# Optimization experiments

Hardware: AMD Instinct MI355X
Metric: run time of the kernel (lower is better)

Reference implementation:

```python
import jax, jax.numpy as jnp
import numpy as np

N, E, IN_C, OUT_C = 100000, 3200000, 128, 32
NEG_SLOPE = 0.2  # PyG GATConv default negative_slope


def setup_inputs() -> dict:
    key = jax.random.key(0)
    ks = jax.random.split(key, 5)
    x = jax.random.normal(ks[0], (N, IN_C), dtype=jnp.float32)
    edge_index = jax.random.randint(ks[1], (2, E), 0, N, dtype=jnp.int32)
    W = jax.random.normal(ks[2], (IN_C, OUT_C), dtype=jnp.float32) * (1.0 / np.sqrt(IN_C))
    att_src = jax.random.normal(ks[3], (OUT_C,), dtype=jnp.float32) * 0.1
    att_dst = jax.random.normal(ks[4], (OUT_C,), dtype=jnp.float32) * 0.1
    bias = jnp.zeros((OUT_C,), dtype=jnp.float32)
    return {"x": x, "edge_index": edge_index, "W": W,
            "att_src": att_src, "att_dst": att_dst, "bias": bias}


def reference(x, edge_index, W, att_src, att_dst, bias):
    # GATConv (heads=1, concat=True, add_self_loops=True) followed by ReLU.
    n = x.shape[0]
    loops = jnp.arange(n, dtype=edge_index.dtype)
    src = jnp.concatenate([edge_index[0], loops])  # [E+N]
    dst = jnp.concatenate([edge_index[1], loops])  # [E+N]

    h = x @ W                       # [N, C] transformed features
    a_src = h @ att_src             # [N] source attention logits
    a_dst = h @ att_dst             # [N] destination attention logits

    # per-edge unnormalized attention
    e = jax.nn.leaky_relu(a_src[src] + a_dst[dst], NEG_SLOPE)  # [E+N]

    # segment softmax over incoming edges of each destination node
    m = jnp.full((n,), -jnp.inf, dtype=e.dtype).at[dst].max(e)  # per-dst max
    p = jnp.exp(e - m[dst])
    denom = jax.ops.segment_sum(p, dst, num_segments=n)
    alpha = p / denom[dst]          # [E+N]

    # scatter-aggregate weighted messages
    out = jax.ops.segment_sum(alpha[:, None] * h[src], dst, num_segments=n)  # [N, C]
    out = jax.nn.relu(out + bias)
    return (out, edge_index)
```

## Files before the change

kernel.cpp:

```cpp
#include <hip/hip_runtime.h>

#define IN_C 128
#define OUT_C 32
#define NEG_SLOPE 0.2f

#define NBUK 512
#define DRANGE 256
#define STILE 8192
#define HST (STILE / 2)
#define CAP 8192
#define RPT (CAP / 1024)

#define GR 128
#define KC 32

typedef _Float16 f16x4 __attribute__((ext_vector_type(4)));
typedef float f32x4 __attribute__((ext_vector_type(4)));

__device__ __forceinline__ unsigned short f16bits(float f) {
    _Float16 h = (_Float16)f;
    unsigned short b;
    __builtin_memcpy(&b, &h, 2);
    return b;
}
__device__ __forceinline__ float f16val(unsigned short b) {
    _Float16 h;
    __builtin_memcpy(&h, &b, 2);
    return (float)h;
}

__device__ __forceinline__ int wave_iscan(int v, int lane) {
    #pragma unroll
    for (int off = 1; off < 64; off <<= 1) {
        int u = __shfl_up(v, off, 64);
        if (lane >= off) v += u;
    }
    return v;
}

__device__ __forceinline__ int bucket_of(int d, unsigned long long M64) {
    return (int)__umul64hi((unsigned long long)d << 9, M64);
}
__device__ __forceinline__ int bucket_lo(int b, int N) {
    return (b * N + (NBUK - 1)) >> 9;
}

__global__ __launch_bounds__(512) void front_kernel(
    const float* __restrict__ x, const float* __restrict__ W,
    const float* __restrict__ att_src, const float* __restrict__ att_dst,
    _Float16* __restrict__ h, float* __restrict__ a_src, float* __restrict__ a_dst,
    const int* __restrict__ ei, int* __restrict__ bcursor,
    unsigned* __restrict__ packed, float* __restrict__ outEcho,
    int N, int E, int nRadix, unsigned long long M64)
{
    extern __shared__ char smem[];
    const int tid = threadIdx.x;
    const int bid = blockIdx.x;

    if (bid < nRadix) {
        int* lcnt = (int*)smem;
        int* sc   = lcnt + NBUK;
        int* gbase = sc + NBUK;
        int* wsum  = gbase + NBUK;
        unsigned* reorder = (unsigned*)(wsum + 8);
        unsigned short* bkt = (unsigned short*)(reorder + HST);

        const int T = E + N;
        const int i0 = bid * STILE;
        const int n = min(STILE, T - i0);

        lcnt[tid] = 0;
        __syncthreads();

        unsigned srcld[STILE / 512];
        unsigned br[STILE / 512];
        #pragma unroll
        for (int j = 0; j < STILE / 512; ++j) {
            int k = tid + j * 512;
            br[j] = 0xFFFFFFFFu;
            if (k < n) {
                int i = i0 + k;
                int s, d;
                if (i < E) {
                    s = ei[i]; d = ei[E + i];
                    __builtin_nontemporal_store((float)s, &outEcho[i]);
                    __builtin_nontemporal_store((float)d, &outEcho[E + i]);
                } else { s = d = i - E; }
                int b = bucket_of(d, M64);
                int local = d - bucket_lo(b, N);
                int r = atomicAdd(&lcnt[b], 1);
                srcld[j] = ((unsigned)s << 8) | (unsigned)local;
                br[j] = ((unsigned)b << 13) | (unsigned)r;
            }
        }
        __syncthreads();

        const int lane = tid & 63, w = tid >> 6;
        int t = lcnt[tid];
        int incl = wave_iscan(t, lane);
        if (lane == 63) wsum[w] = incl;
        __syncthreads();
        if (tid < 8) {
            int orig = wsum[tid];
            int s8 = orig;
            #pragma unroll
            for (int off = 1; off < 8; off <<= 1) {
                int u = __shfl_up(s8, off, 64);
                if (tid >= off) s8 += u;
            }
            wsum[tid] = s8 - orig;
        }
        __syncthreads();
        int ex = wsum[w] + incl - t;
        sc[tid] = ex;
        if (t > 0) gbase[tid] = tid * CAP + atomicAdd(&bcursor[tid], t);
        __syncthreads();

        #pragma unroll
        for (int half = 0; half < 2; ++half) {
            const int base = half * HST;
            #pragma unroll
            for (int j = 0; j < STILE / 512; ++j) {
                if (br[j] != 0xFFFFFFFFu) {
                    unsigned b = br[j] >> 13;
                    unsigned r = br[j] & 0x1FFFu;
                    unsigned p = (unsigned)sc[b] + r;
                    if ((int)(p >> 12) == half) {
                        reorder[p - base] = srcld[j];
                        bkt[p - base] = (unsigned short)b;
                    }
                }
            }
            __syncthreads();
            int hi = n - base;
            if (hi > HST) hi = HST;
            for (int k = tid; k < hi; k += 512) {
                unsigned b = bkt[k];
                int pos = gbase[b] + (base + k - sc[b]);
                if (pos < (int)((b + 1) * CAP)) packed[pos] = reorder[k];
            }
            __syncthreads();
        }
    } else {
        float* wl = (float*)smem;
        float (*xl)[KC + 4] = (float(*)[KC + 4])(smem + IN_C * OUT_C * 4);

        const int rg = tid >> 3;
        const int cg = tid & 7;
        const int r0 = (bid - nRadix) * GR;

        for (int i = tid * 4; i < IN_C * OUT_C; i += 512 * 4)
            *(float4*)&wl[i] = *(const float4*)&W[i];

        float acc[2][4] = {};

        for (int kc = 0; kc < IN_C; kc += KC) {
            __syncthreads();
            for (int s = tid; s < GR * (KC / 4); s += 512) {
                int row = s >> 3, kq = (s & 7) * 4;
                float4 v = make_float4(0.f, 0.f, 0.f, 0.f);
                if (r0 + row < N)
                    v = *(const float4*)&x[(size_t)(r0 + row) * IN_C + kc + kq];
                *(float4*)&xl[row][kq] = v;
            }
            __syncthreads();

            #pragma unroll
            for (int kk = 0; kk < KC; kk += 4) {
                float4 xv[2], wv[4];
                #pragma unroll
                for (int rr = 0; rr < 2; ++rr)
                    xv[rr] = *(float4*)&xl[rg * 2 + rr][kk];
                #pragma unroll
                for (int q = 0; q < 4; ++q)
                    wv[q] = *(float4*)&wl[(kc + kk + q) * OUT_C + cg * 4];
                #pragma unroll
                for (int rr = 0; rr < 2; ++rr) {
                    const float xs[4] = {xv[rr].x, xv[rr].y, xv[rr].z, xv[rr].w};
                    #pragma unroll
                    for (int q = 0; q < 4; ++q) {
                        acc[rr][0] = fmaf(xs[q], wv[q].x, acc[rr][0]);
                        acc[rr][1] = fmaf(xs[q], wv[q].y, acc[rr][1]);
                        acc[rr][2] = fmaf(xs[q], wv[q].z, acc[rr][2]);
                        acc[rr][3] = fmaf(xs[q], wv[q].w, acc[rr][3]);
                    }
                }
            }
        }

        const float4 asv = *(const float4*)&att_src[cg * 4];
        const float4 adv = *(const float4*)&att_dst[cg * 4];

        #pragma unroll
        for (int rr = 0; rr < 2; ++rr) {
            int row = r0 + rg * 2 + rr;
            float ps = acc[rr][0] * asv.x + acc[rr][1] * asv.y
                     + acc[rr][2] * asv.z + acc[rr][3] * asv.w;
            float pd = acc[rr][0] * adv.x + acc[rr][1] * adv.y
                     + acc[rr][2] * adv.z + acc[rr][3] * adv.w;
            ps += __shfl_xor(ps, 4, 8); ps += __shfl_xor(ps, 2, 8); ps += __shfl_xor(ps, 1, 8);
            pd += __shfl_xor(pd, 4, 8); pd += __shfl_xor(pd, 2, 8); pd += __shfl_xor(pd, 1, 8);
            if (row < N) {
                f16x4 hv = {(_Float16)acc[rr][0], (_Float16)acc[rr][1],
                            (_Float16)acc[rr][2], (_Float16)acc[rr][3]};
                *(f16x4*)&h[(size_t)row * OUT_C + cg * 4] = hv;
                if (cg == 0) { a_src[row] = ps; a_dst[row] = pd; }
            }
        }
    }
}

__global__ __launch_bounds__(1024) void sort_agg(
    const unsigned* __restrict__ packed, const int* __restrict__ bcursor,
    const float* __restrict__ a_src, const float* __restrict__ a_dst,
    const _Float16* __restrict__ h, const float* __restrict__ bias,
    float* __restrict__ out, int N)
{
    __shared__ unsigned esL[CAP];
    __shared__ int cnt[DRANGE];
    __shared__ int sc[DRANGE];
    __shared__ int exb[DRANGE];
    __shared__ float adst[DRANGE];
    __shared__ int wsum[4];
    const int tid = threadIdx.x;
    const int b = blockIdx.x;
    const size_t b0 = (size_t)b * CAP;
    const int lo = bucket_lo(b, N);
    const int hi = bucket_lo(b + 1, N);
    const int range = hi - lo;
    int total = bcursor[b];
    if (total > CAP) total = CAP;

    if (tid < DRANGE) {
        cnt[tid] = 0;
        adst[tid] = (tid < range) ? a_dst[lo + tid] : 0.f;
    }
    __syncthreads();

    unsigned pkReg[RPT];
    int rReg[RPT];
    #pragma unroll
    for (int j = 0; j < RPT; ++j) {
        int k = tid + j * 1024;
        rReg[j] = -1;
        if (k < total) {
            unsigned pk = __builtin_nontemporal_load(&packed[b0 + k]);
            pkReg[j] = pk;
            rReg[j] = atomicAdd(&cnt[pk & 255u], 1);
        }
    }
    __syncthreads();

    {
        const int lane = tid & 63, w = tid >> 6;
        int t = (tid < DRANGE) ? cnt[tid] : 0;
        int incl = wave_iscan(t, lane);
        if (tid < DRANGE && lane == 63) wsum[w] = incl;
        __syncthreads();
        if (tid < 4) {
            int orig = wsum[tid];
            int s4 = orig;
            #pragma unroll
            for (int off = 1; off < 4; off <<= 1) {
                int u = __shfl_up(s4, off, 64);
                if (tid >= off) s4 += u;
            }
            wsum[tid] = s4 - orig;
        }
        __syncthreads();
        if (tid < DRANGE) {
            int inclTot = wsum[w] + incl;
            sc[tid] = inclTot;
            exb[tid] = inclTot - t;
        }
    }
    __syncthreads();

    #pragma unroll
    for (int j = 0; j < RPT; ++j) {
        if (rReg[j] >= 0) {
            unsigned pk = pkReg[j];
            int ld = pk & 255u;
            int s  = (int)(pk >> 8);
            float v = a_src[s] + adst[ld];
            v = v > 0.f ? v : NEG_SLOPE * v;
            float p = __expf(v);
            esL[exb[ld] + rReg[j]] = ((unsigned)s << 15) | f16bits(p);
        }
    }
    __syncthreads();

    const int grp  = tid >> 3;
    const int lane = tid & 7;
    const float4 bq = *(const float4*)&bias[lane * 4];

    #pragma unroll
    for (int dd = 0; dd < 2; ++dd) {
        const int ld = grp * 2 + dd;
        const int begin = exb[ld];
        const int end   = sc[ld];
        float a0 = 0.f, a1 = 0.f, a2 = 0.f, a3 = 0.f, dsum = 0.f;
        #pragma unroll 8
        for (int i = begin; i < end; ++i) {
            unsigned pj = esL[i];
            float p = f16val((unsigned short)(pj & 0x7FFFu));
            int   s = (int)(pj >> 15);
            f16x4 hv = *(const f16x4*)&h[(size_t)s * OUT_C + lane * 4];
            dsum += p;
            a0 = fmaf(p, (float)hv.x, a0);
            a1 = fmaf(p, (float)hv.y, a1);
            a2 = fmaf(p, (float)hv.z, a2);
            a3 = fmaf(p, (float)hv.w, a3);
        }
        if (ld < range) {
            int gd = lo + ld;
            float inv = 1.f / dsum;
            float v0 = a0 * inv + bq.x;
            float v1 = a1 * inv + bq.y;
            float v2 = a2 * inv + bq.z;
            float v3 = a3 * inv + bq.w;
            v0 = v0 > 0.f ? v0 : 0.f;
            v1 = v1 > 0.f ? v1 : 0.f;
            v2 = v2 > 0.f ? v2 : 0.f;
            v3 = v3 > 0.f ? v3 : 0.f;
            f32x4 res = {v0, v1, v2, v3};
            __builtin_nontemporal_store(res, (f32x4*)&out[(size_t)gd * OUT_C + lane * 4]);
        }
    }
}

extern "C" void kernel_launch(void* const* d_in, const int* in_sizes, int n_in,
                              void* d_out, int out_size, void* d_ws, size_t ws_size,
                              hipStream_t stream)
{
    const float* x       = (const float*)d_in[0];
    const int*   ei      = (const int*)d_in[1];
    const float* W       = (const float*)d_in[2];
    const float* att_src = (const float*)d_in[3];
    const float* att_dst = (const float*)d_in[4];
    const float* bias    = (const float*)d_in[5];

    const int N = in_sizes[0] / IN_C;
    const int E = in_sizes[1] / 2;
    const int T = E + N;
    const int nRadix = (T + STILE - 1) / STILE;
    const int nGemm  = (N + GR - 1) / GR;

    const unsigned long long M64 = 0xFFFFFFFFFFFFFFFFull / (unsigned)N + 1;

    char* base = (char*)d_ws;
    size_t off = 0;
    _Float16* h = (_Float16*)(base + off);  off += (size_t)N * OUT_C * 2;
    float* a_src = (float*)(base + off);    off += (size_t)N * 4;
    float* a_dst = (float*)(base + off);    off += (size_t)N * 4;
    int* bcursor = (int*)(base + off);      off += (size_t)NBUK * 4;
    unsigned* packed = (unsigned*)(base + off); off += (size_t)NBUK * CAP * 4;

    float* outF = (float*)d_out;

    hipMemsetAsync(bcursor, 0, (size_t)NBUK * 4, stream);

    const int ldsRadix = 3 * NBUK * 4 + 32 + HST * 4 + HST * 2;
    const int ldsGemm  = IN_C * OUT_C * 4 + GR * (KC + 4) * 4;
    const int ldsBytes = ldsRadix > ldsGemm ? ldsRadix : ldsGemm;
    front_kernel<<<nRadix + nGemm, 512, ldsBytes, stream>>>(
        x, W, att_src, att_dst, h, a_src, a_dst,
        ei, bcursor, packed, outF + (size_t)N * OUT_C, N, E, nRadix, M64);

    sort_agg<<<NBUK, 1024, 0, stream>>>(packed, bcursor, a_src, a_dst, h, bias, outF, N);
}
```

Measured before the change: 87.22 us.

## Split h into two 16-channel halves and gather each half in separate passes

The transformed feature table h is stored as two separate half-width arrays (channels 0-15 and 16-31). The aggregation kernel now gathers the first half for both destinations, then the second half, with each lane loading 4 bytes instead of 8. The intent is to shrink the random-gather working set per pass (3.2 MB instead of 6.4 MB), so it fits better in cache and the hit rate on source-row gathers improves. In exchange, each edge's LDS entry is read and decoded twice, and twice as many gather instructions are issued.

```diff
diff --git a/kernel.cpp b/kernel.cpp
--- a/kernel.cpp
+++ b/kernel.cpp
@@ -15,7 +15,8 @@
 #define KC 32
 
 typedef _Float16 f16x4 __attribute__((ext_vector_type(4)));
-typedef float f32x4 __attribute__((ext_vector_type(4)));
+typedef _Float16 f16x2 __attribute__((ext_vector_type(2)));
+typedef float f32x2 __attribute__((ext_vector_type(2)));
 
 __device__ __forceinline__ unsigned short f16bits(float f) {
     _Float16 h = (_Float16)f;
@@ -48,7 +49,8 @@
 __global__ __launch_bounds__(512) void front_kernel(
     const float* __restrict__ x, const float* __restrict__ W,
     const float* __restrict__ att_src, const float* __restrict__ att_dst,
-    _Float16* __restrict__ h, float* __restrict__ a_src, float* __restrict__ a_dst,
+    _Float16* __restrict__ hA, _Float16* __restrict__ hB,
+    float* __restrict__ a_src, float* __restrict__ a_dst,
     const int* __restrict__ ei, int* __restrict__ bcursor,
     unsigned* __restrict__ packed, float* __restrict__ outEcho,
     int N, int E, int nRadix, unsigned long long M64)
@@ -203,7 +205,8 @@
             if (row < N) {
                 f16x4 hv = {(_Float16)acc[rr][0], (_Float16)acc[rr][1],
                             (_Float16)acc[rr][2], (_Float16)acc[rr][3]};
-                *(f16x4*)&h[(size_t)row * OUT_C + cg * 4] = hv;
+                if (cg < 4) *(f16x4*)&hA[(size_t)row * 16 + cg * 4] = hv;
+                else        *(f16x4*)&hB[(size_t)row * 16 + (cg - 4) * 4] = hv;
                 if (cg == 0) { a_src[row] = ps; a_dst[row] = pd; }
             }
         }
@@ -213,8 +216,8 @@
 __global__ __launch_bounds__(1024) void sort_agg(
     const unsigned* __restrict__ packed, const int* __restrict__ bcursor,
     const float* __restrict__ a_src, const float* __restrict__ a_dst,
-    const _Float16* __restrict__ h, const float* __restrict__ bias,
-    float* __restrict__ out, int N)
+    const _Float16* __restrict__ hA, const _Float16* __restrict__ hB,
+    const float* __restrict__ bias, float* __restrict__ out, int N)
 {
     __shared__ unsigned esL[CAP];
     __shared__ int cnt[DRANGE];
@@ -292,40 +295,76 @@
 
     const int grp  = tid >> 3;
     const int lane = tid & 7;
-    const float4 bq = *(const float4*)&bias[lane * 4];
-
-    #pragma unroll
-    for (int dd = 0; dd < 2; ++dd) {
-        const int ld = grp * 2 + dd;
-        const int begin = exb[ld];
-        const int end   = sc[ld];
-        float a0 = 0.f, a1 = 0.f, a2 = 0.f, a3 = 0.f, dsum = 0.f;
-        #pragma unroll 8
-        for (int i = begin; i < end; ++i) {
-            unsigned pj = esL[i];
-            float p = f16val((unsigned short)(pj & 0x7FFFu));
-            int   s = (int)(pj >> 15);
-            f16x4 hv = *(const f16x4*)&h[(size_t)s * OUT_C + lane * 4];
-            dsum += p;
-            a0 = fmaf(p, (float)hv.x, a0);
-            a1 = fmaf(p, (float)hv.y, a1);
-            a2 = fmaf(p, (float)hv.z, a2);
-            a3 = fmaf(p, (float)hv.w, a3);
-        }
-        if (ld < range) {
-            int gd = lo + ld;
-            float inv = 1.f / dsum;
-            float v0 = a0 * inv + bq.x;
-            float v1 = a1 * inv + bq.y;
-            float v2 = a2 * inv + bq.z;
-            float v3 = a3 * inv + bq.w;
-            v0 = v0 > 0.f ? v0 : 0.f;
-            v1 = v1 > 0.f ? v1 : 0.f;
-            v2 = v2 > 0.f ? v2 : 0.f;
-            v3 = v3 > 0.f ? v3 : 0.f;
-            f32x4 res = {v0, v1, v2, v3};
-            __builtin_nontemporal_store(res, (f32x4*)&out[(size_t)gd * OUT_C + lane * 4]);
-        }
+    const int ld0 = grp * 2, ld1 = grp * 2 + 1;
+    const int b00 = exb[ld0], e00 = sc[ld0];
+    const int b01 = exb[ld1], e01 = sc[ld1];
+
+    float a00 = 0.f, a01 = 0.f, d0 = 0.f;
+    float a10 = 0.f, a11 = 0.f, d1 = 0.f;
+    #pragma unroll 8
+    for (int i = b00; i < e00; ++i) {
+        unsigned pj = esL[i];
+        float p = f16val((unsigned short)(pj & 0x7FFFu));
+        int   s = (int)(pj >> 15);
+        f16x2 hv = *(const f16x2*)&hA[(size_t)s * 16 + lane * 2];
+        d0 += p;
+        a00 = fmaf(p, (float)hv.x, a00);
+        a01 = fmaf(p, (float)hv.y, a01);
+    }
+    #pragma unroll 8
+    for (int i = b01; i < e01; ++i) {
+        unsigned pj = esL[i];
+        float p = f16val((unsigned short)(pj & 0x7FFFu));
+        int   s = (int)(pj >> 15);
+        f16x2 hv = *(const f16x2*)&hA[(size_t)s * 16 + lane * 2];
+        d1 += p;
+        a10 = fmaf(p, (float)hv.x, a10);
+        a11 = fmaf(p, (float)hv.y, a11);
+    }
+    float c00 = 0.f, c01 = 0.f, c10 = 0.f, c11 = 0.f;
+    #pragma unroll 8
+    for (int i = b00; i < e00; ++i) {
+        unsigned pj = esL[i];
+        float p = f16val((unsigned short)(pj & 0x7FFFu));
+        int   s = (int)(pj >> 15);
+        f16x2 hv = *(const f16x2*)&hB[(size_t)s * 16 + lane * 2];
+        c00 = fmaf(p, (float)hv.x, c00);
+        c01 = fmaf(p, (float)hv.y, c01);
+    }
+    #pragma unroll 8
+    for (int i = b01; i < e01; ++i) {
+        unsigned pj = esL[i];
+        float p = f16val((unsigned short)(pj & 0x7FFFu));
+        int   s = (int)(pj >> 15);
+        f16x2 hv = *(const f16x2*)&hB[(size_t)s * 16 + lane * 2];
+        c10 = fmaf(p, (float)hv.x, c10);
+        c11 = fmaf(p, (float)hv.y, c11);
+    }
+
+    const float2 bqA = *(const float2*)&bias[lane * 2];
+    const float2 bqB = *(const float2*)&bias[16 + lane * 2];
+
+    if (ld0 < range) {
+        int gd = lo + ld0;
+        float inv = 1.f / d0;
+        float v0 = a00 * inv + bqA.x, v1 = a01 * inv + bqA.y;
+        float v2 = c00 * inv + bqB.x, v3 = c01 * inv + bqB.y;
+        v0 = v0 > 0.f ? v0 : 0.f;  v1 = v1 > 0.f ? v1 : 0.f;
+        v2 = v2 > 0.f ? v2 : 0.f;  v3 = v3 > 0.f ? v3 : 0.f;
+        f32x2 rA = {v0, v1}, rB = {v2, v3};
+        __builtin_nontemporal_store(rA, (f32x2*)&out[(size_t)gd * OUT_C + lane * 2]);
+        __builtin_nontemporal_store(rB, (f32x2*)&out[(size_t)gd * OUT_C + 16 + lane * 2]);
+    }
+    if (ld1 < range) {
+        int gd = lo + ld1;
+        float inv = 1.f / d1;
+        float v0 = a10 * inv + bqA.x, v1 = a11 * inv + bqA.y;
+        float v2 = c10 * inv + bqB.x, v3 = c11 * inv + bqB.y;
+        v0 = v0 > 0.f ? v0 : 0.f;  v1 = v1 > 0.f ? v1 : 0.f;
+        v2 = v2 > 0.f ? v2 : 0.f;  v3 = v3 > 0.f ? v3 : 0.f;
+        f32x2 rA = {v0, v1}, rB = {v2, v3};
+        __builtin_nontemporal_store(rA, (f32x2*)&out[(size_t)gd * OUT_C + lane * 2]);
+        __builtin_nontemporal_store(rB, (f32x2*)&out[(size_t)gd * OUT_C + 16 + lane * 2]);
     }
 }
 
@@ -350,7 +389,8 @@
 
     char* base = (char*)d_ws;
     size_t off = 0;
-    _Float16* h = (_Float16*)(base + off);  off += (size_t)N * OUT_C * 2;
+    _Float16* hA = (_Float16*)(base + off); off += (size_t)N * 16 * 2;
+    _Float16* hB = (_Float16*)(base + off); off += (size_t)N * 16 * 2;
     float* a_src = (float*)(base + off);    off += (size_t)N * 4;
     float* a_dst = (float*)(base + off);    off += (size_t)N * 4;
     int* bcursor = (int*)(base + off);      off += (size_t)NBUK * 4;
@@ -364,8 +404,8 @@
     const int ldsGemm  = IN_C * OUT_C * 4 + GR * (KC + 4) * 4;
     const int ldsBytes = ldsRadix > ldsGemm ? ldsRadix : ldsGemm;
     front_kernel<<<nRadix + nGemm, 512, ldsBytes, stream>>>(
-        x, W, att_src, att_dst, h, a_src, a_dst,
+        x, W, att_src, att_dst, hA, hB, a_src, a_dst,
         ei, bcursor, packed, outF + (size_t)N * OUT_C, N, E, nRadix, M64);
 
-    sort_agg<<<NBUK, 1024, 0, stream>>>(packed, bcursor, a_src, a_dst, h, bias, outF, N);
-}
+    sort_agg<<<NBUK, 1024, 0, stream>>>(packed, bcursor, a_src, a_dst, hA, hB, bias, outF, N);
+}
```

Result: slower. 96.82 us (+11.0%).
